# Performance work log

Hardware: AMD Instinct MI355X
Metric: run time of the kernel (lower is better)

The kernel has to match this reference:

```python
import jax, jax.numpy as jnp
import numpy as np

NC = 80          # num_classes
REG_MAX = 16
TOPK = 10
IMG = 640
STRIDES = (8, 16, 32)
EPS = 1e-9


def make_anchors(shapes, strides):
    pts, strs = [], []
    for (h, w), s in zip(shapes, strides):
        sx = jnp.arange(w, dtype=jnp.float32)  # grid_cell_offset = 0.0
        sy = jnp.arange(h, dtype=jnp.float32)
        gy, gx = jnp.meshgrid(sy, sx, indexing='ij')
        pts.append(jnp.stack([gx, gy], -1).reshape(-1, 2))
        strs.append(jnp.full((h * w, 1), float(s), dtype=jnp.float32))
    return jnp.concatenate(pts, 0), jnp.concatenate(strs, 0)  # [A,2], [A,1]


def ciou(box1, box2, eps=1e-7):
    # boxes are xyxy, broadcastable; returns CIoU with last dim squeezed
    b1x1, b1y1, b1x2, b1y2 = jnp.split(box1, 4, -1)
    b2x1, b2y1, b2x2, b2y2 = jnp.split(box2, 4, -1)
    w1, h1 = b1x2 - b1x1, b1y2 - b1y1
    w2, h2 = b2x2 - b2x1, b2y2 - b2y1
    inter = (jnp.clip(jnp.minimum(b1x2, b2x2) - jnp.maximum(b1x1, b2x1), 0.0)
             * jnp.clip(jnp.minimum(b1y2, b2y2) - jnp.maximum(b1y1, b2y1), 0.0))
    union = w1 * h1 + w2 * h2 - inter + eps
    iou = inter / union
    cw = jnp.maximum(b1x2, b2x2) - jnp.minimum(b1x1, b2x1)
    ch = jnp.maximum(b1y2, b2y2) - jnp.minimum(b1y1, b2y1)
    c2 = cw ** 2 + ch ** 2 + eps
    rho2 = ((b2x1 + b2x2 - b1x1 - b1x2) ** 2 + (b2y1 + b2y2 - b1y1 - b1y2) ** 2) / 4.0
    v = (4.0 / np.pi ** 2) * (jnp.arctan(w2 / (h2 + eps)) - jnp.arctan(w1 / (h1 + eps))) ** 2
    alpha = jax.lax.stop_gradient(v / (v - iou + (1.0 + eps)))
    return (iou - (rho2 / c2 + v * alpha))[..., 0]


def bbox_decode(anchor_points, pred_distri):
    # distribution-focal decode: softmax over REG_MAX bins, expectation, dist2bbox
    B, A, _ = pred_distri.shape
    pd = pred_distri.reshape(B, A, 4, REG_MAX)
    proj = jnp.arange(REG_MAX, dtype=jnp.float32)
    dist = jnp.einsum('bacr,r->bac', jax.nn.softmax(pd, -1), proj)  # [B,A,4] ltrb
    lt, rb = dist[..., :2], dist[..., 2:]
    return jnp.concatenate([anchor_points - lt, anchor_points + rb], -1)  # xyxy


def assigner(pd_scores, pd_bboxes, anc_points, gt_labels, gt_bboxes, mask_gt,
             alpha=0.5, beta=6.0):
    # pd_scores [B,A,C] (sigmoid), pd_bboxes [B,A,4], gt_* [B,M,...], mask_gt [B,M,1]
    B, A, C = pd_scores.shape
    M = gt_bboxes.shape[1]
    mask_gt = mask_gt.astype(jnp.float32)
    # anchors whose center lies inside each gt box
    lt = anc_points[None, None, :, :] - gt_bboxes[:, :, None, :2]   # [B,M,A,2]
    rb = gt_bboxes[:, :, None, 2:] - anc_points[None, None, :, :]
    mask_in_gts = (jnp.minimum(lt.min(-1), rb.min(-1)) > EPS).astype(jnp.float32)  # [B,M,A]
    mask = mask_in_gts * mask_gt
    # class score of each anchor at the gt's label
    sc = jnp.take_along_axis(pd_scores[:, None, :, :],
                             gt_labels[:, :, None, None].astype(jnp.int32), axis=-1)[..., 0]  # [B,M,A]
    overlaps = jnp.clip(ciou(gt_bboxes[:, :, None, :], pd_bboxes[:, None, :, :]), 0.0) * mask
    bbox_scores = sc * mask
    align_metric = (bbox_scores ** alpha) * (overlaps ** beta)  # [B,M,A]
    # top-k candidates per gt
    _, idxs = jax.lax.top_k(align_metric, TOPK)                 # [B,M,K]
    valid = jnp.broadcast_to(mask_gt > 0, (B, M, TOPK))
    idxs = jnp.where(valid, idxs, 0)
    cnt = jnp.zeros((B * M, A), jnp.float32).at[
        jnp.arange(B * M)[:, None], idxs.reshape(B * M, TOPK)
    ].add(valid.reshape(B * M, TOPK).astype(jnp.float32)).reshape(B, M, A)
    mask_topk = jnp.where(cnt > 1, 0.0, cnt)
    mask_pos = mask_topk * mask_in_gts * mask_gt               # [B,M,A]
    # resolve anchors assigned to multiple gts by max overlap
    fg = mask_pos.sum(1)                                       # [B,A]
    multi = fg[:, None, :] > 1
    is_max = jax.nn.one_hot(overlaps.argmax(1), M, dtype=jnp.float32).transpose(0, 2, 1)
    mask_pos = jnp.where(multi, is_max, mask_pos)
    fg_mask = mask_pos.sum(1)                                  # [B,A]
    tgt_idx = mask_pos.argmax(1)                               # [B,A]
    # gather targets
    flat = tgt_idx + jnp.arange(B)[:, None] * M
    t_labels = jnp.clip(gt_labels.reshape(-1)[flat], 0)        # [B,A]
    t_bboxes = gt_bboxes.reshape(-1, 4)[flat]                  # [B,A,4]
    t_scores = jax.nn.one_hot(t_labels, C, dtype=jnp.float32) * (fg_mask[..., None] > 0)
    # normalize scores by aligned metric
    am = align_metric * mask_pos
    pos_am = am.max(-1, keepdims=True)                         # [B,M,1]
    pos_ov = (overlaps * mask_pos).max(-1, keepdims=True)      # [B,M,1]
    norm = (am * pos_ov / (pos_am + EPS)).max(1)[..., None]    # [B,A,1]
    return t_bboxes, t_scores * norm, fg_mask > 0


def setup_inputs() -> dict:
    key = jax.random.key(0)
    ks = jax.random.split(key, 9)
    B, M = 16, 32
    inp = {
        'cls0': jax.random.normal(ks[0], (B, NC, 80, 80), jnp.float32),
        'cls1': jax.random.normal(ks[1], (B, NC, 40, 40), jnp.float32),
        'cls2': jax.random.normal(ks[2], (B, NC, 20, 20), jnp.float32),
        'reg0': jax.random.normal(ks[3], (B, 4 * REG_MAX, 80, 80), jnp.float32),
        'reg1': jax.random.normal(ks[4], (B, 4 * REG_MAX, 40, 40), jnp.float32),
        'reg2': jax.random.normal(ks[5], (B, 4 * REG_MAX, 20, 20), jnp.float32),
    }
    cxy = jax.random.uniform(ks[6], (B, M, 2), minval=0.1, maxval=0.9)
    wh = jax.random.uniform(ks[7], (B, M, 2), minval=0.02, maxval=0.25)
    inp['boxes'] = jnp.concatenate([cxy, wh], -1)  # normalized cxcywh
    inp['labels'] = jax.random.randint(ks[8], (B, M), 0, NC)
    return inp


def reference(cls0, cls1, cls2, reg0, reg1, reg2, boxes, labels):
    cls_out, reg_out = [cls0, cls1, cls2], [reg0, reg1, reg2]
    B = cls0.shape[0]
    anc, stride_t = make_anchors([r.shape[2:] for r in reg_out], STRIDES)
    pred_scores = jnp.concatenate(
        [c.transpose(0, 2, 3, 1).reshape(B, -1, NC) for c in cls_out], 1)        # [B,A,C]
    pred_distri = jnp.concatenate(
        [r.transpose(0, 2, 3, 1).reshape(B, -1, 4 * REG_MAX) for r in reg_out], 1)
    # gt2xyxy: normalized cxcywh -> pixel xyxy
    cx, cy, w, h = jnp.split(boxes, 4, -1)
    gt_bboxes = jnp.concatenate([(cx - w / 2) * IMG, (cy - h / 2) * IMG,
                                 (cx + w / 2) * IMG, (cy + h / 2) * IMG], -1)
    mask_gt = gt_bboxes.sum(2, keepdims=True) > 0.0
    pred_bboxes = bbox_decode(anc, pred_distri)                                   # anchor units
    sg = jax.lax.stop_gradient
    t_bboxes, t_scores, fg_mask = assigner(
        sg(jax.nn.sigmoid(pred_scores)), sg(pred_bboxes) * stride_t,
        anc * stride_t, labels, gt_bboxes, mask_gt)
    tss = jnp.maximum(t_scores.sum(), 1.0)
    # classification BCE-with-logits
    x, t = pred_scores, t_scores
    bce = jnp.maximum(x, 0.0) - x * t + jnp.log1p(jnp.exp(-jnp.abs(x)))
    l_cls = bce.sum() / tss
    # bbox CIoU loss
    t_bboxes = t_bboxes / stride_t
    weight = t_scores.sum(-1) * fg_mask                                           # [B,A]
    iou = ciou(pred_bboxes, t_bboxes)
    l_iou = ((1.0 - iou) * weight).sum() / tss
    # DFL loss
    tltrb = jnp.clip(jnp.concatenate([anc - t_bboxes[..., :2],
                                      t_bboxes[..., 2:] - anc], -1),
                     0.0, REG_MAX - 1 - 0.01)                                     # [B,A,4]
    logp = jax.nn.log_softmax(pred_distri.reshape(B, -1, 4, REG_MAX), -1)
    tl = jnp.floor(tltrb).astype(jnp.int32)
    wl = (tl + 1).astype(jnp.float32) - tltrb
    lp_tl = jnp.take_along_axis(logp, tl[..., None], -1)[..., 0]
    lp_tr = jnp.take_along_axis(logp, (tl + 1)[..., None], -1)[..., 0]
    dfl = (-(lp_tl * wl + lp_tr * (1.0 - wl))).mean(-1)                           # [B,A]
    l_dfl = (dfl * weight).sum() / tss
    loss = jnp.stack([0.5 * l_cls, 7.5 * l_iou, 1.5 * l_dfl])
    return loss.sum(), loss
```

## Files before the change

kernel.cpp:

```cpp
#include <hip/hip_runtime.h>

#define NB 16
#define NM 32
#define NA 8400
#define NCC 80
#define NREG 64
#define A0 6400
#define A1 1600
#define A2 400
#define CAP 768

#define PRE_GRID 1024
#define PL_GRID 525


__device__ __forceinline__ void anch(int a, float& ax, float& ay, float& s, int& lvl, int& p) {
  if (a < A0)            { lvl = 0; p = a;          s = 8.f;  ax = (float)(p % 80); ay = (float)(p / 80); }
  else if (a < A0 + A1)  { lvl = 1; p = a - A0;     s = 16.f; ax = (float)(p % 40); ay = (float)(p / 40); }
  else                   { lvl = 2; p = a - A0 - A1; s = 32.f; ax = (float)(p % 20); ay = (float)(p / 20); }
}

__device__ __forceinline__ float cls_at(const float* c0, const float* c1, const float* c2,
                                        int b, int ch, int a) {
  if (a < A0)           return c0[((size_t)(b * NCC + ch)) * A0 + a];
  if (a < A0 + A1)      return c1[((size_t)(b * NCC + ch)) * A1 + (a - A0)];
  return c2[((size_t)(b * NCC + ch)) * A2 + (a - A0 - A1)];
}

__device__ __forceinline__ float reg_at(const float* r0, const float* r1, const float* r2,
                                        int b, int ch, int lvl, int p) {
  if (lvl == 0) return r0[((size_t)(b * NREG + ch)) * A0 + p];
  if (lvl == 1) return r1[((size_t)(b * NREG + ch)) * A1 + p];
  return r2[((size_t)(b * NREG + ch)) * A2 + p];
}

__device__ __forceinline__ void gtbox(const float* boxes, int b, int m,
                                      float& x1, float& y1, float& x2, float& y2, bool& valid) {
  const float* q = boxes + ((size_t)(b * NM + m)) * 4;
  float cx = q[0], cy = q[1], w = q[2], h = q[3];
  x1 = (cx - w * 0.5f) * 640.f; y1 = (cy - h * 0.5f) * 640.f;
  x2 = (cx + w * 0.5f) * 640.f; y2 = (cy + h * 0.5f) * 640.f;
  valid = (x1 + y1 + x2 + y2) > 0.f;
}

__device__ __forceinline__ float ciou_f(float b1x1, float b1y1, float b1x2, float b1y2,
                                        float b2x1, float b2y1, float b2x2, float b2y2) {
  const float eps = 1e-7f;
  float w1 = b1x2 - b1x1, h1 = b1y2 - b1y1;
  float w2 = b2x2 - b2x1, h2 = b2y2 - b2y1;
  float iw = fmaxf(fminf(b1x2, b2x2) - fmaxf(b1x1, b2x1), 0.f);
  float ih = fmaxf(fminf(b1y2, b2y2) - fmaxf(b1y1, b2y1), 0.f);
  float inter = iw * ih;
  float uni = w1 * h1 + w2 * h2 - inter + eps;
  float iou = inter / uni;
  float cw = fmaxf(b1x2, b2x2) - fminf(b1x1, b2x1);
  float ch = fmaxf(b1y2, b2y2) - fminf(b1y1, b2y1);
  float c2 = cw * cw + ch * ch + eps;
  float dx = b2x1 + b2x2 - b1x1 - b1x2;
  float dy = b2y1 + b2y2 - b1y1 - b1y2;
  float rho2 = (dx * dx + dy * dy) * 0.25f;
  float at = atanf(w2 / (h2 + eps)) - atanf(w1 / (h1 + eps));
  float v = 0.4052847345693511f * at * at;
  float alpha = v / (v - iou + (1.0f + eps));
  return iou - (rho2 / c2 + v * alpha);
}

__device__ __forceinline__ float align_of(float sc, float o) {
  float o2 = o * o, o4 = o2 * o2;
  return sqrtf(sc) * (o2 * o4);
}

__device__ __forceinline__ float softplus_fast(float x) {
  float e = __expf(-fabsf(x));
  return fmaxf(x, 0.f) + __logf(1.f + e);
}


__global__ __launch_bounds__(256) void k_pre(
    const float* r0, const float* r1, const float* r2,
    const float* c0, const float* c1, const float* c2,
    float4* bb, float4* mls, int* fgcnt, int* msum,
    unsigned* pos_am, unsigned* pos_ov, double* gt_acc, double* bce_part) {
  const int gtid = blockIdx.x * 256 + threadIdx.x;
  const int nthr = gridDim.x * 256;

  for (int t = gtid; t < NB * NA; t += nthr) { fgcnt[t] = 0; msum[t] = 0; }
  if (gtid < NB * NM) { pos_am[gtid] = 0u; pos_ov[gtid] = 0u; }
  if (gtid < NB * NM * 4) gt_acc[gtid] = 0.0;

  for (int q = gtid; q < (NB * NA) / 2; q += nthr) {
    int t0 = q * 2;
    int b = t0 / NA, a0 = t0 % NA;
    float ax0, ay, s; int lvl, p0;
    anch(a0, ax0, ay, s, lvl, p0);
    const float* rg; int HW;
    if (lvl == 0) { rg = r0; HW = A0; }
    else if (lvl == 1) { rg = r1; HW = A1; }
    else { rg = r2; HW = A2; }
    const float* base = rg + ((size_t)b * NREG) * HW + p0;
    float dist[4][2], ml[4][2];
#pragma unroll
    for (int sd = 0; sd < 4; ++sd) {
      float mx0 = -1e30f, mx1 = -1e30f;
      float se0 = 0.f, se1 = 0.f, ws0 = 0.f, ws1 = 0.f;
      for (int r = 0; r < 16; ++r) {
        float2 v = *(const float2*)(base + (size_t)(sd * 16 + r) * HW);
        float fr = (float)r;
        float nm0 = fmaxf(mx0, v.x);
        float rs0 = __expf(mx0 - nm0);
        float e0  = __expf(v.x - nm0);
        se0 = se0 * rs0 + e0; ws0 = ws0 * rs0 + e0 * fr; mx0 = nm0;
        float nm1 = fmaxf(mx1, v.y);
        float rs1 = __expf(mx1 - nm1);
        float e1  = __expf(v.y - nm1);
        se1 = se1 * rs1 + e1; ws1 = ws1 * rs1 + e1 * fr; mx1 = nm1;
      }
      dist[sd][0] = ws0 / se0;  ml[sd][0] = mx0 + __logf(se0);
      dist[sd][1] = ws1 / se1;  ml[sd][1] = mx1 + __logf(se1);
    }
#pragma unroll
    for (int j = 0; j < 2; ++j) {
      float axj = ax0 + (float)j;
      bb[t0 + j]  = make_float4(axj - dist[0][j], ay - dist[1][j], axj + dist[2][j], ay + dist[3][j]);
      mls[t0 + j] = make_float4(ml[0][j], ml[1][j], ml[2][j], ml[3][j]);
    }
  }

  const size_t N0 = (size_t)NB * NCC * A0 / 4;
  const size_t N1 = (size_t)NB * NCC * A1 / 4;
  const size_t N2 = (size_t)NB * NCC * A2 / 4;
  const size_t NT = N0 + N1 + N2;
  const float4* f0 = (const float4*)c0;
  const float4* f1 = (const float4*)c1;
  const float4* f2 = (const float4*)c2;
  float s0 = 0.f, s1 = 0.f;
  for (size_t i = (size_t)gtid; i < NT; i += (size_t)nthr) {
    float4 v;
    if (i < N0) v = f0[i];
    else if (i < N0 + N1) v = f1[i - N0];
    else v = f2[i - N0 - N1];
    s0 += softplus_fast(v.x) + softplus_fast(v.z);
    s1 += softplus_fast(v.y) + softplus_fast(v.w);
  }
  __shared__ double sred[256];
  sred[threadIdx.x] = (double)(s0 + s1);
  __syncthreads();
  for (int off = 128; off; off >>= 1) {
    if (threadIdx.x < off) sred[threadIdx.x] += sred[threadIdx.x + off];
    __syncthreads();
  }
  if (threadIdx.x == 0) bce_part[blockIdx.x] = sred[0];
}


__global__ __launch_bounds__(256) void k_assign(
    const float* boxes, const int* labels, const float4* bb,
    const float* c0, const float* c1, const float* c2,
    int* fgcnt, int* msum) {
  __shared__ float sv[CAP];
  __shared__ int   si[CAP];
  __shared__ int   s_n;
  const int bm = blockIdx.x;
  const int b = bm / NM, m = bm % NM;
  const int tid = threadIdx.x;
  const int lane = tid & 63;

  float gx1, gy1, gx2, gy2; bool valid;
  gtbox(boxes, b, m, gx1, gy1, gx2, gy2, valid);
  if (!valid) return;
  int lbl = labels[bm]; if (lbl < 0) lbl = 0; if (lbl >= NCC) lbl = NCC - 1;
  if (tid == 0) s_n = 0;
  __syncthreads();

  const int   Ws[3]   = {80, 40, 20};
  const float ss[3]   = {8.f, 16.f, 32.f};
  const int   loff[3] = {0, A0, A0 + A1};
  int rx0[3], ry0[3], rw[3], bc[3];
  int total = 0;
  for (int l = 0; l < 3; ++l) {
    float s = ss[l]; int W = Ws[l];
    int ax0 = (int)floorf((gx1 + 1e-9f) / s);
    int ax1 = (int)ceilf((gx2 - 1e-9f) / s);
    int ay0 = (int)floorf((gy1 + 1e-9f) / s);
    int ay1 = (int)ceilf((gy2 - 1e-9f) / s);
    ax0 = max(ax0, 0); ay0 = max(ay0, 0);
    ax1 = min(ax1, W - 1); ay1 = min(ay1, W - 1);
    rx0[l] = ax0; ry0[l] = ay0;
    rw[l] = max(0, ax1 - ax0 + 1);
    int rhl = max(0, ay1 - ay0 + 1);
    bc[l] = total;
    total += rw[l] * rhl;
  }
  int iters = (total + 255) >> 8;
  for (int it = 0; it < iters; ++it) {
    int idx = it * 256 + tid;
    bool pred = false; float am = 0.f; int a = 0;
    if (idx < total) {
      int l = (idx >= bc[2]) ? 2 : ((idx >= bc[1]) ? 1 : 0);
      int r = idx - bc[l];
      int iy = r / rw[l], ix = r - iy * rw[l];
      int axg = rx0[l] + ix, ayg = ry0[l] + iy;
      a = loff[l] + ayg * Ws[l] + axg;
      float s = ss[l];
      float axp = (float)axg * s, ayp = (float)ayg * s;
      float mn = fminf(fminf(axp - gx1, ayp - gy1), fminf(gx2 - axp, gy2 - ayp));
      if (mn > 1e-9f) {
        pred = true;
        float4 pb = bb[(size_t)b * NA + a];
        float c = ciou_f(gx1, gy1, gx2, gy2, pb.x * s, pb.y * s, pb.z * s, pb.w * s);
        float o = fmaxf(c, 0.f);
        float x = cls_at(c0, c1, c2, b, lbl, a);
        float sc = 1.f / (1.f + expf(-x));
        am = align_of(sc, o);
      }
    }
    unsigned long long mask = __ballot(pred);
    if (mask) {
      int nact = __popcll(mask);
      int leader = __ffsll(mask) - 1;
      int basec = 0;
      if (lane == leader) basec = atomicAdd(&s_n, nact);
      basec = __shfl(basec, leader);
      if (pred) {
        int off = basec + __popcll(mask & ((1ull << lane) - 1ull));
        if (off < CAP) { sv[off] = am; si[off] = a; }
      }
    }
  }
  __syncthreads();
  int n = s_n; if (n > CAP) n = CAP;
  if (n == 0) return;
  if (tid >= 64) return;

  float v[12]; int ix[12];
#pragma unroll
  for (int k = 0; k < 12; ++k) {
    int j = k * 64 + tid;
    bool in = (j < n);
    v[k]  = in ? sv[j] : -2.f;
    ix[k] = in ? si[j] : (1 << 30);
  }
  int cnt = 0;
#pragma unroll
  for (int k = 0; k < 12; ++k) cnt += (v[k] > 0.f) ? 1 : 0;
  for (int o = 32; o; o >>= 1) cnt += __shfl_xor(cnt, o);
  int npos = cnt;

  if (npos > 10) {
    for (int p = 0; p < 10; ++p) {
      float bv = -1.f; int bi = 1 << 30;
#pragma unroll
      for (int k = 0; k < 12; ++k) {
        if (v[k] > bv || (v[k] == bv && ix[k] < bi)) { bv = v[k]; bi = ix[k]; }
      }
      for (int o = 32; o; o >>= 1) {
        float wv = __shfl_xor(bv, o); int wi = __shfl_xor(bi, o);
        if (wv > bv || (wv == bv && wi < bi)) { bv = wv; bi = wi; }
      }
#pragma unroll
      for (int k = 0; k < 12; ++k) if (ix[k] == bi) v[k] = -1.f;
      if (tid == 0) {
        atomicAdd(&fgcnt[(size_t)b * NA + bi], 1);
        atomicAdd(&msum[(size_t)b * NA + bi], m);
      }
    }
  } else {
#pragma unroll
    for (int k = 0; k < 12; ++k) {
      if (v[k] > 0.f) {
        atomicAdd(&fgcnt[(size_t)b * NA + ix[k]], 1);
        atomicAdd(&msum[(size_t)b * NA + ix[k]], m);
      }
    }
    int need = 10 - npos;
    for (int j = tid; j < n; j += 64) {
      if (sv[j] == 0.f) {
        int i = si[j];
        if (i < 10) {
          int pb = 0;
          for (int q = 0; q < n; ++q) pb += (sv[q] > 0.f && si[q] < i) ? 1 : 0;
          if (i - pb < need) {
            atomicAdd(&fgcnt[(size_t)b * NA + i], 1);
            atomicAdd(&msum[(size_t)b * NA + i], m);
          }
        }
      }
    }
  }
}


__global__ __launch_bounds__(256) void k_rp(
    const float* boxes, const int* labels,
    const float4* bb, const float4* mls,
    const float* c0, const float* c1, const float* c2,
    const float* r0, const float* r1, const float* r2,
    const int* fgcnt, const int* msum,
    unsigned* pos_am, unsigned* pos_ov, double* gt_acc) {
  int t = blockIdx.x * 256 + threadIdx.x;
  if (t >= NB * NA) return;
  int fg = fgcnt[t];
  if (fg == 0) return;
  int b = t / NA, a = t % NA;
  float ax, ay, s; int lvl, p;
  anch(a, ax, ay, s, lvl, p);
  float axp = ax * s, ayp = ay * s;
  float4 pb = bb[t];
  float px1 = pb.x * s, py1 = pb.y * s, px2 = pb.z * s, py2 = pb.w * s;
  int asn; float o;
  if (fg == 1) {
    asn = msum[t];
    float gx1, gy1, gx2, gy2; bool valid;
    gtbox(boxes, b, asn, gx1, gy1, gx2, gy2, valid);
    o = fmaxf(ciou_f(gx1, gy1, gx2, gy2, px1, py1, px2, py2), 0.f);
  } else {
    float bv = -1e30f; int bi = 0;
    for (int m = 0; m < NM; ++m) {
      float gx1, gy1, gx2, gy2; bool valid;
      gtbox(boxes, b, m, gx1, gy1, gx2, gy2, valid);
      float om = 0.f;
      if (valid) {
        float mn = fminf(fminf(axp - gx1, ayp - gy1), fminf(gx2 - axp, gy2 - ayp));
        if (mn > 1e-9f)
          om = fmaxf(ciou_f(gx1, gy1, gx2, gy2, px1, py1, px2, py2), 0.f);
      }
      if (om > bv) { bv = om; bi = m; }
    }
    asn = bi; o = bv;
  }
  if (o <= 0.f) return;
  int g = b * NM + asn;
  int lbl = labels[g]; if (lbl < 0) lbl = 0; if (lbl >= NCC) lbl = NCC - 1;
  float x = cls_at(c0, c1, c2, b, lbl, a);
  float sc = 1.f / (1.f + expf(-x));
  float am = align_of(sc, o);
  atomicMax(&pos_am[g], __float_as_uint(am));
  atomicMax(&pos_ov[g], __float_as_uint(o));
  if (am <= 0.f) return;

  float gx1, gy1, gx2, gy2; bool valid;
  gtbox(boxes, b, asn, gx1, gy1, gx2, gy2, valid);
  float inv_s = 1.f / s;
  float tx1 = gx1 * inv_s, ty1 = gy1 * inv_s, tx2 = gx2 * inv_s, ty2 = gy2 * inv_s;
  float iou = ciou_f(pb.x, pb.y, pb.z, pb.w, tx1, ty1, tx2, ty2);
  float4 ml = mls[t];
  float tgt[4] = { ax - tx1, ay - ty1, tx2 - ax, ty2 - ay };
  float mlv[4] = { ml.x, ml.y, ml.z, ml.w };
  float dfl = 0.f;
  for (int sd = 0; sd < 4; ++sd) {
    float tv = fminf(fmaxf(tgt[sd], 0.f), 14.99f);
    float tlf = floorf(tv);
    int tl = (int)tlf;
    float wl = (tlf + 1.f) - tv;
    float xtl = reg_at(r0, r1, r2, b, sd * 16 + tl,     lvl, p);
    float xtr = reg_at(r0, r1, r2, b, sd * 16 + tl + 1, lvl, p);
    dfl += -((xtl - mlv[sd]) * wl + (xtr - mlv[sd]) * (1.f - wl));
  }
  dfl *= 0.25f;
  atomicAdd(&gt_acc[g * 4 + 0], (double)am);
  atomicAdd(&gt_acc[g * 4 + 1], (double)(am * x));
  atomicAdd(&gt_acc[g * 4 + 2], (double)(am * (1.f - iou)));
  atomicAdd(&gt_acc[g * 4 + 3], (double)(am * dfl));
}


__global__ __launch_bounds__(256) void k_final(const double* bce_part, const double* gt_acc,
                                               const unsigned* pos_am, const unsigned* pos_ov,
                                               float* out) {
  const int tid = threadIdx.x;
  double tss = 0.0, sx = 0.0, siou = 0.0, sdfl = 0.0, bce = 0.0;
  for (int g = tid; g < NB * NM; g += 256) {
    float pam = __uint_as_float(pos_am[g]);
    float pov = __uint_as_float(pos_ov[g]);
    double sc = (double)pov / ((double)pam + 1e-9);
    tss  += gt_acc[g * 4 + 0] * sc;
    sx   += gt_acc[g * 4 + 1] * sc;
    siou += gt_acc[g * 4 + 2] * sc;
    sdfl += gt_acc[g * 4 + 3] * sc;
  }
  for (int i = tid; i < PRE_GRID; i += 256) bce += bce_part[i];
  __shared__ double sred[256];
  double vals[5] = { tss, sx, siou, sdfl, bce };
  double tot[5];
  for (int q = 0; q < 5; ++q) {
    sred[tid] = vals[q];
    __syncthreads();
    for (int off = 128; off; off >>= 1) {
      if (tid < off) sred[tid] += sred[tid + off];
      __syncthreads();
    }
    tot[q] = sred[0];
    __syncthreads();
  }
  if (tid == 0) {
    double t = tot[0]; if (t < 1.0) t = 1.0;
    double l0 = 0.5 * (tot[4] - tot[1]) / t;
    double l1 = 7.5 * tot[2] / t;
    double l2 = 1.5 * tot[3] / t;
    out[0] = (float)(l0 + l1 + l2);
    out[1] = (float)l0;
    out[2] = (float)l1;
    out[3] = (float)l2;
  }
}


extern "C" void kernel_launch(void* const* d_in, const int* in_sizes, int n_in,
                              void* d_out, int out_size, void* d_ws, size_t ws_size,
                              hipStream_t stream) {
  (void)in_sizes; (void)n_in; (void)out_size; (void)ws_size;
  const float* cls0  = (const float*)d_in[0];
  const float* cls1  = (const float*)d_in[1];
  const float* cls2  = (const float*)d_in[2];
  const float* reg0  = (const float*)d_in[3];
  const float* reg1  = (const float*)d_in[4];
  const float* reg2  = (const float*)d_in[5];
  const float* boxes = (const float*)d_in[6];
  const int*   labels = (const int*)d_in[7];
  float* out = (float*)d_out;

  const size_t BA = (size_t)NB * NA;
  const int    BM = NB * NM;

  char* wsb = (char*)d_ws;
  double*   bce_part = (double*)wsb;
  double*   gt_acc   = bce_part + PRE_GRID;
  unsigned* pos_am   = (unsigned*)(gt_acc + (size_t)BM * 4);
  unsigned* pos_ov   = pos_am + BM;
  int*      fgcnt    = (int*)(pos_ov + BM);
  int*      msum     = fgcnt + BA;
  float*    bbp      = (float*)(msum + BA);
  float*    mlsp     = bbp + BA * 4;

  float4* bb  = (float4*)bbp;
  float4* mls = (float4*)mlsp;

  k_pre<<<PRE_GRID, 256, 0, stream>>>(reg0, reg1, reg2, cls0, cls1, cls2,
                                      bb, mls, fgcnt, msum, pos_am, pos_ov,
                                      gt_acc, bce_part);
  k_assign<<<BM, 256, 0, stream>>>(boxes, labels, (const float4*)bb,
                                   cls0, cls1, cls2, fgcnt, msum);
  k_rp<<<PL_GRID, 256, 0, stream>>>(boxes, labels, (const float4*)bb, (const float4*)mls,
                                    cls0, cls1, cls2, reg0, reg1, reg2,
                                    fgcnt, msum, pos_am, pos_ov, gt_acc);
  k_final<<<1, 256, 0, stream>>>(bce_part, gt_acc, pos_am, pos_ov, out);
}
```

Measured before the change: 67.57 us.

## Split preprocessing into per-side decode kernel and separate BCE reduction kernel

The fused pre-kernel is split in two. A decode kernel uses one thread per (side, anchor), giving 4x more threads, and does a two-pass softmax over 16 bins preloaded into registers. The BCE softplus reduction becomes its own kernel launched after k_rp, so it is no longer on the path to assignment. This adds a kernel launch and uses scalar strided stores for the box and log-sum outputs instead of float4 stores.

```diff
diff --git a/kernel.cpp b/kernel.cpp
--- a/kernel.cpp
+++ b/kernel.cpp
@@ -10,7 +10,8 @@
 #define A2 400
 #define CAP 768
 
-#define PRE_GRID 1024
+#define DEC_GRID 2100
+#define BCE_GRID 1024
 #define PL_GRID 525
 
 
@@ -76,65 +77,57 @@
 }
 
 
-__global__ __launch_bounds__(256) void k_pre(
+__global__ __launch_bounds__(256) void k_decode(
     const float* r0, const float* r1, const float* r2,
-    const float* c0, const float* c1, const float* c2,
-    float4* bb, float4* mls, int* fgcnt, int* msum,
-    unsigned* pos_am, unsigned* pos_ov, double* gt_acc, double* bce_part) {
-  const int gtid = blockIdx.x * 256 + threadIdx.x;
-  const int nthr = gridDim.x * 256;
-
-  for (int t = gtid; t < NB * NA; t += nthr) { fgcnt[t] = 0; msum[t] = 0; }
-  if (gtid < NB * NM) { pos_am[gtid] = 0u; pos_ov[gtid] = 0u; }
-  if (gtid < NB * NM * 4) gt_acc[gtid] = 0.0;
-
-  for (int q = gtid; q < (NB * NA) / 2; q += nthr) {
-    int t0 = q * 2;
-    int b = t0 / NA, a0 = t0 % NA;
-    float ax0, ay, s; int lvl, p0;
-    anch(a0, ax0, ay, s, lvl, p0);
-    const float* rg; int HW;
-    if (lvl == 0) { rg = r0; HW = A0; }
-    else if (lvl == 1) { rg = r1; HW = A1; }
-    else { rg = r2; HW = A2; }
-    const float* base = rg + ((size_t)b * NREG) * HW + p0;
-    float dist[4][2], ml[4][2];
-#pragma unroll
-    for (int sd = 0; sd < 4; ++sd) {
-      float mx0 = -1e30f, mx1 = -1e30f;
-      float se0 = 0.f, se1 = 0.f, ws0 = 0.f, ws1 = 0.f;
-      for (int r = 0; r < 16; ++r) {
-        float2 v = *(const float2*)(base + (size_t)(sd * 16 + r) * HW);
-        float fr = (float)r;
-        float nm0 = fmaxf(mx0, v.x);
-        float rs0 = __expf(mx0 - nm0);
-        float e0  = __expf(v.x - nm0);
-        se0 = se0 * rs0 + e0; ws0 = ws0 * rs0 + e0 * fr; mx0 = nm0;
-        float nm1 = fmaxf(mx1, v.y);
-        float rs1 = __expf(mx1 - nm1);
-        float e1  = __expf(v.y - nm1);
-        se1 = se1 * rs1 + e1; ws1 = ws1 * rs1 + e1 * fr; mx1 = nm1;
-      }
-      dist[sd][0] = ws0 / se0;  ml[sd][0] = mx0 + __logf(se0);
-      dist[sd][1] = ws1 / se1;  ml[sd][1] = mx1 + __logf(se1);
-    }
-#pragma unroll
-    for (int j = 0; j < 2; ++j) {
-      float axj = ax0 + (float)j;
-      bb[t0 + j]  = make_float4(axj - dist[0][j], ay - dist[1][j], axj + dist[2][j], ay + dist[3][j]);
-      mls[t0 + j] = make_float4(ml[0][j], ml[1][j], ml[2][j], ml[3][j]);
-    }
-  }
-
+    float* bbf, float* mlsf, int* fgcnt, int* msum,
+    unsigned* pos_am, unsigned* pos_ov, double* gt_acc) {
+  const int g = blockIdx.x * 256 + threadIdx.x;
+  if (g < NB * NA) { fgcnt[g] = 0; msum[g] = 0; }
+  if (g < NB * NM) { pos_am[g] = 0u; pos_ov[g] = 0u; }
+  if (g < NB * NM * 4) gt_acc[g] = 0.0;
+
+  const int BA = NB * NA;
+  const int sd = g / BA;
+  const int t  = g - sd * BA;
+  int b = t / NA, a = t - (t / NA) * NA;
+  float ax, ay, s; int lvl, p;
+  anch(a, ax, ay, s, lvl, p);
+  const float* rg; int HW;
+  if (lvl == 0) { rg = r0; HW = A0; }
+  else if (lvl == 1) { rg = r1; HW = A1; }
+  else { rg = r2; HW = A2; }
+  const float* base = rg + ((size_t)(b * NREG + sd * 16)) * HW + p;
+  float xv[16];
+#pragma unroll
+  for (int r = 0; r < 16; ++r) xv[r] = base[(size_t)r * HW];
+  float mx = xv[0];
+#pragma unroll
+  for (int r = 1; r < 16; ++r) mx = fmaxf(mx, xv[r]);
+  float se = 0.f, ws = 0.f;
+#pragma unroll
+  for (int r = 0; r < 16; ++r) { float e = __expf(xv[r] - mx); se += e; ws += e * (float)r; }
+  float dist = ws / se;
+  float ml = mx + __logf(se);
+  float v;
+  if (sd == 0)      v = ax - dist;
+  else if (sd == 1) v = ay - dist;
+  else if (sd == 2) v = ax + dist;
+  else              v = ay + dist;
+  bbf[(size_t)t * 4 + sd]  = v;
+  mlsf[(size_t)t * 4 + sd] = ml;
+}
+
+
+__global__ __launch_bounds__(256) void k_bce(const float4* f0, const float4* f1, const float4* f2,
+                                             double* bce_part) {
   const size_t N0 = (size_t)NB * NCC * A0 / 4;
   const size_t N1 = (size_t)NB * NCC * A1 / 4;
   const size_t N2 = (size_t)NB * NCC * A2 / 4;
   const size_t NT = N0 + N1 + N2;
-  const float4* f0 = (const float4*)c0;
-  const float4* f1 = (const float4*)c1;
-  const float4* f2 = (const float4*)c2;
+  const size_t i0 = (size_t)blockIdx.x * 256 + threadIdx.x;
+  const size_t stride = (size_t)gridDim.x * 256;
   float s0 = 0.f, s1 = 0.f;
-  for (size_t i = (size_t)gtid; i < NT; i += (size_t)nthr) {
+  for (size_t i = i0; i < NT; i += stride) {
     float4 v;
     if (i < N0) v = f0[i];
     else if (i < N0 + N1) v = f1[i - N0];
@@ -378,7 +371,7 @@
     siou += gt_acc[g * 4 + 2] * sc;
     sdfl += gt_acc[g * 4 + 3] * sc;
   }
-  for (int i = tid; i < PRE_GRID; i += 256) bce += bce_part[i];
+  for (int i = tid; i < BCE_GRID; i += 256) bce += bce_part[i];
   __shared__ double sred[256];
   double vals[5] = { tss, sx, siou, sdfl, bce };
   double tot[5];
@@ -424,7 +417,7 @@
 
   char* wsb = (char*)d_ws;
   double*   bce_part = (double*)wsb;
-  double*   gt_acc   = bce_part + PRE_GRID;
+  double*   gt_acc   = bce_part + BCE_GRID;
   unsigned* pos_am   = (unsigned*)(gt_acc + (size_t)BM * 4);
   unsigned* pos_ov   = pos_am + BM;
   int*      fgcnt    = (int*)(pos_ov + BM);
@@ -435,13 +428,14 @@
   float4* bb  = (float4*)bbp;
   float4* mls = (float4*)mlsp;
 
-  k_pre<<<PRE_GRID, 256, 0, stream>>>(reg0, reg1, reg2, cls0, cls1, cls2,
-                                      bb, mls, fgcnt, msum, pos_am, pos_ov,
-                                      gt_acc, bce_part);
+  k_decode<<<DEC_GRID, 256, 0, stream>>>(reg0, reg1, reg2, bbp, mlsp,
+                                         fgcnt, msum, pos_am, pos_ov, gt_acc);
   k_assign<<<BM, 256, 0, stream>>>(boxes, labels, (const float4*)bb,
                                    cls0, cls1, cls2, fgcnt, msum);
   k_rp<<<PL_GRID, 256, 0, stream>>>(boxes, labels, (const float4*)bb, (const float4*)mls,
                                     cls0, cls1, cls2, reg0, reg1, reg2,
                                     fgcnt, msum, pos_am, pos_ov, gt_acc);
+  k_bce<<<BCE_GRID, 256, 0, stream>>>((const float4*)cls0, (const float4*)cls1, (const float4*)cls2,
+                                      bce_part);
   k_final<<<1, 256, 0, stream>>>(bce_part, gt_acc, pos_am, pos_ov, out);
 }
```

Measured after the change: 67.49 us. About the same (-0.1%).
